# Kernel tuning notes

Hardware: AMD Instinct MI355X
Metric: run time of the kernel (lower is better)

The kernel has to match this reference:

```python
import jax, jax.numpy as jnp
import numpy as np

B, L, T = 32, 512, 400
EMB, PRE, ENC, ARNN, DRNN, NSYM = 512, 256, 512, 1024, 1024, 256
MEAN_COEFF, SCALE_COEFF = 1.0, 10.0


def setup_inputs() -> dict:
    key = jax.random.key(0)
    ks = jax.random.split(key, 20)
    s = 0.02
    inp = {
        'memory': jax.random.normal(ks[0], (B, L, ENC), jnp.float32),
        'decoder_inputs': jax.random.normal(ks[1], (B, EMB, T), jnp.float32),
        'memory_lengths': jax.random.randint(ks[2], (B,), L // 2, L + 1).astype(jnp.int64),
        # prenet
        'pW1': jax.random.normal(ks[3], (PRE, EMB), jnp.float32) * s,
        'pb1': jnp.zeros((PRE,), jnp.float32),
        'pW2': jax.random.normal(ks[4], (PRE, PRE), jnp.float32) * s,
        'pb2': jnp.zeros((PRE,), jnp.float32),
        # attention LSTMCell
        'aWih': jax.random.normal(ks[5], (4 * ARNN, PRE + ENC), jnp.float32) * s,
        'aWhh': jax.random.normal(ks[6], (4 * ARNN, ARNN), jnp.float32) * s,
        'abih': jnp.zeros((4 * ARNN,), jnp.float32),
        'abhh': jnp.zeros((4 * ARNN,), jnp.float32),
        # Gaussian attention param linear (weight zero-init in torch; small here)
        'attWp': jax.random.normal(ks[7], (2, ARNN), jnp.float32) * 0.001,
        'attbp': jnp.zeros((2,), jnp.float32),
        # decoder LSTMCell
        'dWih': jax.random.normal(ks[8], (4 * DRNN, ARNN + ENC), jnp.float32) * s,
        'dWhh': jax.random.normal(ks[9], (4 * DRNN, DRNN), jnp.float32) * s,
        'dbih': jnp.zeros((4 * DRNN,), jnp.float32),
        'dbhh': jnp.zeros((4 * DRNN,), jnp.float32),
        # output linear
        'oW': jax.random.normal(ks[10], (NSYM, DRNN + ENC), jnp.float32) * s,
        'ob': jnp.zeros((NSYM,), jnp.float32),
    }
    return inp


def _lstm_cell(x, h, c, Wih, Whh, bih, bhh):
    g = x @ Wih.T + bih + h @ Whh.T + bhh
    i, f, gg, o = jnp.split(g, 4, axis=-1)
    c = jax.nn.sigmoid(f) * c + jax.nn.sigmoid(i) * jnp.tanh(gg)
    h = jax.nn.sigmoid(o) * jnp.tanh(c)
    return h, c


def _decoder_core(memory, decoder_inputs, memory_lengths,
                  pW1, pb1, pW2, pb2,
                  aWih, aWhh, abih, abhh,
                  attWp, attbp,
                  dWih, dWhh, dbih, dbhh,
                  oW, ob):
    b = memory.shape[0]
    Lm = memory.shape[1]
    # go frame + time-major inputs -> prenet (dropout is identity in eval)
    x = jnp.transpose(decoder_inputs, (2, 0, 1))            # [T, B, EMB]
    x = jnp.concatenate([jnp.zeros((1, b, EMB), x.dtype), x], axis=0)  # [T+1, B, EMB]
    x = jax.nn.relu(x @ pW1.T + pb1)
    x = jax.nn.relu(x @ pW2.T + pb2)                        # [T+1, B, PRE]
    x = x[:T]                                               # loop runs T steps

    lin = jnp.arange(Lm, dtype=memory.dtype)[None, :]       # [1, L]
    pad_mask = lin >= memory_lengths[:, None].astype(memory.dtype)  # [B, L] True at pad

    def step(carry, x_t):
        ah, ac, dh, dc, ctx, mean = carry
        cell_in = jnp.concatenate([x_t, ctx], axis=1)
        ah, ac = _lstm_cell(cell_in, ah, ac, aWih, aWhh, abih, abhh)
        params = ah @ attWp.T + attbp                       # [B, 2]
        mean = mean + jnp.exp(params[:, 0:1]) * MEAN_COEFF  # [B, 1]
        scale = jnp.exp(params[:, 1:2]) * SCALE_COEFF       # [B, 1]
        Z = jnp.sqrt(2.0 * np.pi * scale ** 2)
        w = jnp.exp(-0.5 * (lin - mean) ** 2 / scale ** 2) / Z  # [B, L]
        w = jnp.where(pad_mask, 0.0, w)
        ctx = jnp.einsum('bl,bld->bd', w, memory)           # [B, ENC]
        dec_in = jnp.concatenate([ah, ctx], axis=1)
        dh, dc = _lstm_cell(dec_in, dh, dc, dWih, dWhh, dbih, dbhh)
        out = jnp.concatenate([dh, ctx], axis=1) @ oW.T + ob  # [B, NSYM]
        return (ah, ac, dh, dc, ctx, mean), (out, w, params)

    z = jnp.zeros
    carry0 = (z((b, ARNN)), z((b, ARNN)), z((b, DRNN)), z((b, DRNN)),
              z((b, ENC)), z((b, 1)))
    _, (logits, aligns, ps) = jax.lax.scan(step, carry0, x)
    # time-major -> [B, T, ...]
    return (jnp.transpose(logits, (1, 0, 2)),
            jnp.transpose(aligns, (1, 0, 2)),
            jnp.transpose(ps, (1, 0, 2)))


def reference(memory, decoder_inputs, memory_lengths,
              pW1, pb1, pW2, pb2,
              aWih, aWhh, abih, abhh,
              attWp, attbp,
              dWih, dWhh, dbih, dbhh,
              oW, ob):
    return _decoder_core(memory, decoder_inputs, memory_lengths,
                         pW1, pb1, pW2, pb2,
                         aWih, aWhh, abih, abhh,
                         attWp, attbp,
                         dWih, dWhh, dbih, dbhh,
                         oW, ob)
```

## Files before the change

kernel.cpp:

```cpp
#include <hip/hip_runtime.h>
#include <math.h>

#define Bsz   32
#define Lmem  512
#define Tsteps 400
#define EMBD  512
#define PRE   256
#define ENCD  512
#define ARNN  1024
#define DRNN  1024
#define NSYM  256

typedef _Float16 f16x8 __attribute__((ext_vector_type(8)));
typedef float    f32x4 __attribute__((ext_vector_type(4)));
typedef _Float16 half_t;

#define KA  (PRE + ENCD + ARNN)
#define KAQ (KA / 4)
#define NMA (KAQ / 32)
#define KD  (ARNN + ENCD + DRNN)
#define KDQ (KD / 4)
#define NMD (KDQ / 32)
#define LDA_A 1800
#define LDA_D 2568

__device__ __forceinline__ void st_agent_f16(half_t* p, half_t v) {
    __hip_atomic_store((unsigned short*)p, __builtin_bit_cast(unsigned short, v),
                       __ATOMIC_RELAXED, __HIP_MEMORY_SCOPE_AGENT);
}
__device__ __forceinline__ void st_agent_f32(float* p, float v) {
    __hip_atomic_store(p, v, __ATOMIC_RELAXED, __HIP_MEMORY_SCOPE_AGENT);
}
__device__ __forceinline__ void st_agent_u32(unsigned* p, unsigned v) {
    __hip_atomic_store(p, v, __ATOMIC_RELAXED, __HIP_MEMORY_SCOPE_AGENT);
}
__device__ __forceinline__ float ld_agent_f32(const float* p) {
    return __hip_atomic_load(p, __ATOMIC_RELAXED, __HIP_MEMORY_SCOPE_AGENT);
}
__device__ __forceinline__ unsigned ld_agent_u32(const unsigned* p) {
    return __hip_atomic_load(p, __ATOMIC_RELAXED, __HIP_MEMORY_SCOPE_AGENT);
}
__device__ __forceinline__ f16x8 ld_agent_f16x8(const half_t* p) {
    union { unsigned long long u[2]; f16x8 v; } c;
    c.u[0] = __hip_atomic_load((const unsigned long long*)p,
                               __ATOMIC_RELAXED, __HIP_MEMORY_SCOPE_AGENT);
    c.u[1] = __hip_atomic_load(((const unsigned long long*)p) + 1,
                               __ATOMIC_RELAXED, __HIP_MEMORY_SCOPE_AGENT);
    return c.v;
}
__device__ __forceinline__ void keep16(f16x8& v) { asm volatile("" : "+v"(v)); }

template<int KIH, int KHH>
__global__ __launch_bounds__(256) void conv_lstm_w(
    const float* __restrict__ Wih, const float* __restrict__ Whh,
    const float* __restrict__ bih, const float* __restrict__ bhh,
    half_t* __restrict__ Wcat, float* __restrict__ bsum)
{
    constexpr int K = KIH + KHH;
    const int j = blockIdx.x;
    const float* srcA = Wih + (size_t)j * KIH;
    const float* srcB = Whh + (size_t)j * KHH;
    half_t* dst = Wcat + (size_t)j * K;
    for (int k = threadIdx.x; k < KIH; k += 256) dst[k]       = (half_t)srcA[k];
    for (int k = threadIdx.x; k < KHH; k += 256) dst[KIH + k] = (half_t)srcB[k];
    if (threadIdx.x == 0) bsum[j] = bih[j] + bhh[j];
}

__global__ __launch_bounds__(256) void conv_mat(
    const float* __restrict__ src, half_t* __restrict__ dst, int n)
{
    for (int i = blockIdx.x * 256 + threadIdx.x; i < n; i += gridDim.x * 256)
        dst[i] = (half_t)src[i];
}

__global__ __launch_bounds__(256) void prenet_kernel(
    const float* __restrict__ din,
    const float* __restrict__ pW1, const float* __restrict__ pb1,
    const float* __restrict__ pW2, const float* __restrict__ pb2,
    half_t* __restrict__ xpre)
{
    __shared__ float xs[8][EMBD];
    __shared__ float h1s[8][PRE];
    const int tid = threadIdx.x;
    const int row0 = blockIdx.x * 8;

    for (int idx = tid; idx < 8 * EMBD; idx += 256) {
        int r = idx >> 9;
        int e = idx & 511;
        int rid = row0 + r;
        int t = rid >> 5;
        int b = rid & 31;
        float v = 0.f;
        if (t > 0) v = din[(size_t)b * EMBD * Tsteps + (size_t)e * Tsteps + (t - 1)];
        xs[r][e] = v;
    }
    __syncthreads();

    {
        float acc[8] = {0.f,0.f,0.f,0.f,0.f,0.f,0.f,0.f};
        const float* wr = pW1 + (size_t)tid * EMBD;
        for (int e = 0; e < EMBD; e += 4) {
            float4 wv = *(const float4*)(wr + e);
            #pragma unroll
            for (int r = 0; r < 8; ++r) {
                float4 xv = *(const float4*)&xs[r][e];
                acc[r] += wv.x * xv.x + wv.y * xv.y + wv.z * xv.z + wv.w * xv.w;
            }
        }
        float bias = pb1[tid];
        #pragma unroll
        for (int r = 0; r < 8; ++r) h1s[r][tid] = fmaxf(acc[r] + bias, 0.f);
    }
    __syncthreads();

    {
        float acc[8] = {0.f,0.f,0.f,0.f,0.f,0.f,0.f,0.f};
        const float* wr = pW2 + (size_t)tid * PRE;
        for (int e = 0; e < PRE; e += 4) {
            float4 wv = *(const float4*)(wr + e);
            #pragma unroll
            for (int r = 0; r < 8; ++r) {
                float4 xv = *(const float4*)&h1s[r][e];
                acc[r] += wv.x * xv.x + wv.y * xv.y + wv.z * xv.z + wv.w * xv.w;
            }
        }
        float bias = pb2[tid];
        #pragma unroll
        for (int r = 0; r < 8; ++r) {
            int rid = row0 + r;
            int t = rid >> 5;
            int b = rid & 31;
            xpre[(size_t)t * Bsz * PRE + (size_t)b * PRE + tid] =
                (half_t)fmaxf(acc[r] + bias, 0.f);
        }
    }
}

__device__ __forceinline__ void g_arrive(unsigned* flags, unsigned ph)
{
    asm volatile("s_waitcnt vmcnt(0)" ::: "memory");
    __syncthreads();
    if (threadIdx.x == 0)
        st_agent_u32(flags + blockIdx.x * 16, ph);
}
__device__ __forceinline__ void g_wait(unsigned* flags, unsigned ph)
{
    if (blockIdx.x < 16 && threadIdx.x < 16) {
        const unsigned* f = flags + (blockIdx.x * 16 + threadIdx.x) * 16;
        while (ld_agent_u32(f) < ph) __builtin_amdgcn_s_sleep(1);
        if (threadIdx.x == 0)
            st_agent_u32(flags + (256 + blockIdx.x) * 16, ph);
    }
    if (blockIdx.x == 0 && threadIdx.x < 16) {
        const unsigned* f2 = flags + (256 + threadIdx.x) * 16;
        while (ld_agent_u32(f2) < ph) __builtin_amdgcn_s_sleep(1);
        if (threadIdx.x == 0)
            st_agent_u32(flags + 272 * 16, ph);
    }
    if (threadIdx.x == 0) {
        const unsigned* g = flags + 272 * 16;
        while (ld_agent_u32(g) < ph) __builtin_amdgcn_s_sleep(1);
    }
    __syncthreads();
}

__global__ __launch_bounds__(512, 1) void decoder_persistent(
    const half_t* __restrict__ Wcat_a, const float* __restrict__ bsum_a,
    const half_t* __restrict__ Wcat_d, const float* __restrict__ bsum_d,
    const half_t* __restrict__ Wo, const float* __restrict__ ob,
    const half_t* __restrict__ xpre,
    const float* __restrict__ attWp, const float* __restrict__ attbp,
    const int* __restrict__ mlen, const half_t* __restrict__ mem16,
    half_t* __restrict__ ah0, half_t* __restrict__ ah1,
    half_t* __restrict__ dh0, half_t* __restrict__ dh1,
    half_t* __restrict__ ctx0, half_t* __restrict__ ctx1,
    float* __restrict__ mean0, float* __restrict__ mean1,
    float* __restrict__ logits, float* __restrict__ aligns,
    float* __restrict__ ps,
    unsigned* flags)
{
    const int blk   = blockIdx.x;
    const int tid   = threadIdx.x;
    const int wave  = tid >> 6;
    const int lane  = tid & 63;
    const int btile = wave & 1;
    const int kq    = wave >> 1;
    const int m15   = lane & 15;
    const int kh    = lane >> 4;
    const int u0    = blk << 2;
    const int bb    = (btile << 4) + m15;

    __shared__ __align__(16) half_t wAl[16 * LDA_A];
    __shared__ __align__(16) half_t wDl[16 * LDA_D];
    __shared__ float gredA[4][2][16][16];
    __shared__ float gredD[4][2][16][16];
    __shared__ float wsh[Lmem];
    __shared__ float lred[16][33];
    __shared__ float wred8[8][2];
    __shared__ float bc2[2];

    for (int g = tid; g < 16 * (KA / 8); g += 512) {
        int r = g / (KA / 8);
        int c = (g - r * (KA / 8)) * 8;
        int jr = (r >> 2) * 1024 + u0 + (r & 3);
        *(f16x8*)(wAl + r * LDA_A + c) = *(const f16x8*)(Wcat_a + (size_t)jr * KA + c);
    }
    for (int g = tid; g < 16 * (KD / 8); g += 512) {
        int r = g / (KD / 8);
        int c = (g - r * (KD / 8)) * 8;
        int jr = (r >> 2) * 1024 + u0 + (r & 3);
        *(f16x8*)(wDl + r * LDA_D + c) = *(const f16x8*)(Wcat_d + (size_t)jr * KD + c);
    }
    float bsA[4] = {0.f,0.f,0.f,0.f}, bsD[4] = {0.f,0.f,0.f,0.f};
    float cA = 0.f, cD = 0.f;
    if (tid < 128) {
        const int ul = tid >> 5;
        #pragma unroll
        for (int gi = 0; gi < 4; ++gi) bsA[gi] = bsum_a[gi * 1024 + u0 + ul];
    } else if (tid < 256) {
        const int ul = (tid - 128) >> 5;
        #pragma unroll
        for (int gi = 0; gi < 4; ++gi) bsD[gi] = bsum_d[gi * 1024 + u0 + ul];
    }
    const half_t* lA = wAl + m15 * LDA_A + kq * KAQ + (kh << 3);
    const half_t* lD = wDl + m15 * LDA_D + kq * KDQ + (kh << 3);
    __syncthreads();

    f16x8 bvA[NMA], bvD[NMD];
    {
        const half_t* s0 = xpre;
        #pragma unroll
        for (int i = 0; i < NMA; ++i) {
            const int kg = kq * KAQ + i * 32 + (kh << 3);
            if (kg < PRE)             bvA[i] = *(const f16x8*)(s0 + bb * PRE + kg);
            else if (kg < PRE + ENCD) bvA[i] = ld_agent_f16x8(ctx1 + bb * ENCD + (kg - PRE));
            else                      bvA[i] = ld_agent_f16x8(ah1 + bb * ARNN + (kg - PRE - ENCD));
        }
    }

    unsigned ph = 0;

    for (int t = 0; t <= Tsteps; ++t) {
        const int par = t & 1;
        half_t*       ah_cur  = par ? ah1 : ah0;
        half_t*       ctx_cur = par ? ctx1 : ctx0;
        const half_t* ctx_prv = par ? ctx0 : ctx1;
        float*        mn_cur  = par ? mean1 : mean0;
        const float*  mn_prv  = par ? mean0 : mean1;
        half_t*       dh_s    = par ? dh0 : dh1;

        if (t < Tsteps) {
            f32x4 accA = {0.f,0.f,0.f,0.f};
            #pragma unroll
            for (int i = 0; i < NMA; ++i) {
                f16x8 av = *(const f16x8*)(lA + i * 32);
                accA = __builtin_amdgcn_mfma_f32_16x16x32_f16(av, bvA[i], accA, 0, 0, 0);
            }
            #pragma unroll
            for (int r = 0; r < 4; ++r)
                gredA[kq][btile][(kh << 2) + r][m15] = accA[r];
        }
        if (t > 0) {
            f32x4 accD = {0.f,0.f,0.f,0.f};
            #pragma unroll
            for (int i = 0; i < NMD; ++i) {
                f16x8 av = *(const f16x8*)(lD + i * 32);
                accD = __builtin_amdgcn_mfma_f32_16x16x32_f16(av, bvD[i], accD, 0, 0, 0);
            }
            #pragma unroll
            for (int r = 0; r < 4; ++r)
                gredD[kq][btile][(kh << 2) + r][m15] = accD[r];
        }
        __syncthreads();
        if (tid < 128) {
            if (t < Tsteps) {
                const int ul = tid >> 5;
                const int bq = tid & 31;
                const int bt = bq >> 4;
                const int nn = bq & 15;
                float g[4];
                #pragma unroll
                for (int gi = 0; gi < 4; ++gi) {
                    const int mr = (gi << 2) + ul;
                    g[gi] = gredA[0][bt][mr][nn] + gredA[1][bt][mr][nn]
                          + gredA[2][bt][mr][nn] + gredA[3][bt][mr][nn] + bsA[gi];
                }
                float si = 1.f / (1.f + expf(-g[0]));
                float sf = 1.f / (1.f + expf(-g[1]));
                float so = 1.f / (1.f + expf(-g[3]));
                cA = sf * cA + si * tanhf(g[2]);
                st_agent_f16(&ah_cur[bq * 1024 + u0 + ul], (half_t)(so * tanhf(cA)));
            }
        } else if (tid < 256) {
            if (t > 0) {
                const int lt = tid - 128;
                const int ul = lt >> 5;
                const int bq = lt & 31;
                const int bt = bq >> 4;
                const int nn = bq & 15;
                float g[4];
                #pragma unroll
                for (int gi = 0; gi < 4; ++gi) {
                    const int mr = (gi << 2) + ul;
                    g[gi] = gredD[0][bt][mr][nn] + gredD[1][bt][mr][nn]
                          + gredD[2][bt][mr][nn] + gredD[3][bt][mr][nn] + bsD[gi];
                }
                float si = 1.f / (1.f + expf(-g[0]));
                float sf = 1.f / (1.f + expf(-g[1]));
                float so = 1.f / (1.f + expf(-g[3]));
                cD = sf * cD + si * tanhf(g[2]);
                st_agent_f16(&dh_s[bq * 1024 + u0 + ul], (half_t)(so * tanhf(cD)));
            }
        }
        ++ph; g_arrive(flags, ph); g_wait(flags, ph);

        if (t < Tsteps) {
            const int abt = blk >> 3;
            const int dt  = blk & 7;
            float p0, p1;
            {
                union { unsigned u; _Float16 h[2]; } a;
                a.u = ld_agent_u32((const unsigned*)(ah_cur + abt * ARNN + 2 * tid));
                float a0 = (float)a.h[0], a1 = (float)a.h[1];
                float2 w0 = *(const float2*)(attWp + 2 * tid);
                float2 w1 = *(const float2*)(attWp + ARNN + 2 * tid);
                p0 = a0 * w0.x + a1 * w0.y;
                p1 = a0 * w1.x + a1 * w1.y;
            }
            #pragma unroll
            for (int off = 32; off > 0; off >>= 1) {
                p0 += __shfl_down(p0, off, 64);
                p1 += __shfl_down(p1, off, 64);
            }
            if (lane == 0) { wred8[wave][0] = p0; wred8[wave][1] = p1; }
            __syncthreads();
            if (tid == 0) {
                float q0 = attbp[0], q1 = attbp[1];
                #pragma unroll
                for (int w = 0; w < 8; ++w) { q0 += wred8[w][0]; q1 += wred8[w][1]; }
                float mn = ld_agent_f32(&mn_prv[abt]) + expf(q0) * 1.0f;
                float sc = expf(q1) * 10.0f;
                if (dt == 0) {
                    st_agent_f32(&mn_cur[abt], mn);
                    st_agent_f32(&ps[(size_t)abt * Tsteps * 2 + (size_t)t * 2 + 0], q0);
                    st_agent_f32(&ps[(size_t)abt * Tsteps * 2 + (size_t)t * 2 + 1], q1);
                }
                bc2[0] = mn; bc2[1] = sc;
            }
            __syncthreads();
            const float mn = bc2[0], sc = bc2[1];
            const float inv_s = 1.f / sc;
            const float coef = 0.3989422804014327f * inv_s;
            const int len = mlen[abt];
            {
                float z = ((float)tid - mn) * inv_s;
                float wv = (tid < len) ? expf(-0.5f * z * z) * coef : 0.f;
                wsh[tid] = wv;
                if (dt == 0)
                    st_agent_f32(&aligns[(size_t)abt * Tsteps * Lmem + (size_t)t * Lmem + tid], wv);
            }
            __syncthreads();
            int lo = (int)fmaxf(0.f, floorf(mn - 9.f * sc));
            int hi = (int)fminf((float)len, ceilf(mn + 9.f * sc) + 1.f);
            const int d8 = (dt << 6) + (wave << 3);
            const half_t* mb = mem16 + (size_t)abt * Lmem * ENCD + d8;
            float acc[8] = {0.f,0.f,0.f,0.f,0.f,0.f,0.f,0.f};
            for (int l = lo + lane; l < hi; l += 64) {
                f16x8 mv = *(const f16x8*)(mb + (size_t)l * ENCD);
                float w = wsh[l];
                #pragma unroll
                for (int j = 0; j < 8; ++j) acc[j] += w * (float)mv[j];
            }
            #pragma unroll
            for (int off = 32; off > 0; off >>= 1) {
                #pragma unroll
                for (int j = 0; j < 8; ++j) acc[j] += __shfl_down(acc[j], off, 64);
            }
            if (lane == 0) {
                #pragma unroll
                for (int j = 0; j < 4; ++j) {
                    union { unsigned u; _Float16 h[2]; } pk;
                    pk.h[0] = (_Float16)acc[2 * j];
                    pk.h[1] = (_Float16)acc[2 * j + 1];
                    st_agent_u32((unsigned*)(ctx_cur + abt * ENCD + d8 + 2 * j), pk.u);
                }
            }
        }
        if (t > 0) {
            const int b_o = tid & 31;
            const int ks  = tid >> 5;
            const half_t* wrow = Wo + (size_t)blk * (DRNN + ENCD) + ks * 96;
            float outacc = 0.f;
            #pragma unroll
            for (int half = 0; half < 2; ++half) {
                f16x8 wv[6], av[6];
                #pragma unroll
                for (int c8 = 0; c8 < 6; ++c8) {
                    const int cc = half * 6 + c8;
                    const int k = ks * 96 + cc * 8;
                    wv[c8] = *(const f16x8*)(wrow + cc * 8);
                    const half_t* ap = (k < DRNN) ? (dh_s + b_o * DRNN + k)
                                                  : (ctx_prv + b_o * ENCD + (k - DRNN));
                    av[c8] = ld_agent_f16x8(ap);
                }
                #pragma unroll
                for (int c8 = 0; c8 < 6; ++c8)
                    #pragma unroll
                    for (int e = 0; e < 8; ++e)
                        outacc += (float)wv[c8][e] * (float)av[c8][e];
            }
            lred[ks][b_o] = outacc;
            __syncthreads();
            if (tid < 32) {
                float s = 0.f;
                #pragma unroll
                for (int q = 0; q < 16; ++q) s += lred[q][tid];
                st_agent_f32(&logits[(size_t)tid * Tsteps * NSYM + (size_t)(t - 1) * NSYM + blk],
                             s + ob[blk]);
            }
        }
        if (t < Tsteps) {
            ++ph; g_arrive(flags, ph);
            if (t + 1 < Tsteps) {
                const half_t* s0n = xpre + (size_t)(t + 1) * Bsz * PRE;
                #pragma unroll
                for (int i = 0; i < NMA; ++i) {
                    const int kg = kq * KAQ + i * 32 + (kh << 3);
                    if (kg < PRE)
                        bvA[i] = *(const f16x8*)(s0n + bb * PRE + kg);
                    else if (kg >= PRE + ENCD)
                        bvA[i] = ld_agent_f16x8(ah_cur + bb * ARNN + (kg - PRE - ENCD));
                }
            }
            #pragma unroll
            for (int i = 0; i < NMD; ++i) {
                const int kg = kq * KDQ + i * 32 + (kh << 3);
                if (kg < ARNN)
                    bvD[i] = ld_agent_f16x8(ah_cur + bb * ARNN + kg);
                else if (kg >= ARNN + ENCD)
                    bvD[i] = ld_agent_f16x8(dh_s + bb * DRNN + (kg - ARNN - ENCD));
            }
            #pragma unroll
            for (int i = 0; i < NMA; ++i) keep16(bvA[i]);
            #pragma unroll
            for (int i = 0; i < NMD; ++i) keep16(bvD[i]);
            g_wait(flags, ph);
            if (t + 1 < Tsteps) {
                #pragma unroll
                for (int i = 0; i < NMA; ++i) {
                    const int kg = kq * KAQ + i * 32 + (kh << 3);
                    if (kg >= PRE && kg < PRE + ENCD)
                        bvA[i] = ld_agent_f16x8(ctx_cur + bb * ENCD + (kg - PRE));
                }
            }
            #pragma unroll
            for (int i = 0; i < NMD; ++i) {
                const int kg = kq * KDQ + i * 32 + (kh << 3);
                if (kg >= ARNN && kg < ARNN + ENCD)
                    bvD[i] = ld_agent_f16x8(ctx_cur + bb * ENCD + (kg - ARNN));
            }
        }
    }
}

extern "C" void kernel_launch(void* const* d_in, const int* in_sizes, int n_in,
                              void* d_out, int out_size, void* d_ws, size_t ws_size,
                              hipStream_t stream)
{
    (void)in_sizes; (void)n_in; (void)out_size; (void)ws_size;
    const float* memory = (const float*)d_in[0];
    const float* din    = (const float*)d_in[1];
    const int*   mlen   = (const int*)d_in[2];
    const float* pW1    = (const float*)d_in[3];
    const float* pb1    = (const float*)d_in[4];
    const float* pW2    = (const float*)d_in[5];
    const float* pb2    = (const float*)d_in[6];
    const float* aWih   = (const float*)d_in[7];
    const float* aWhh   = (const float*)d_in[8];
    const float* abih   = (const float*)d_in[9];
    const float* abhh   = (const float*)d_in[10];
    const float* attWp  = (const float*)d_in[11];
    const float* attbp  = (const float*)d_in[12];
    const float* dWih   = (const float*)d_in[13];
    const float* dWhh   = (const float*)d_in[14];
    const float* dbih   = (const float*)d_in[15];
    const float* dbhh   = (const float*)d_in[16];
    const float* oW     = (const float*)d_in[17];
    const float* ob     = (const float*)d_in[18];

    float* logits = (float*)d_out;
    float* aligns = logits + (size_t)Bsz * Tsteps * NSYM;
    float* ps     = aligns + (size_t)Bsz * Tsteps * Lmem;

    char* base = (char*)d_ws;
    auto alloc = [&](size_t bytes) -> char* {
        char* p = base; base += (bytes + 255) & ~(size_t)255; return p;
    };
    half_t* Wcat_a = (half_t*)alloc((size_t)4096 * KA * 2);
    half_t* Wcat_d = (half_t*)alloc((size_t)4096 * KD * 2);
    half_t* Wo     = (half_t*)alloc((size_t)NSYM * (DRNN + ENCD) * 2);
    float*  bsum_a = (float*)alloc(4096 * 4);
    float*  bsum_d = (float*)alloc(4096 * 4);
    half_t* xpre   = (half_t*)alloc((size_t)Tsteps * Bsz * PRE * 2);
    half_t* mem16  = (half_t*)alloc((size_t)Bsz * Lmem * ENCD * 2);
    half_t* ah0    = (half_t*)alloc(Bsz * ARNN * 2);
    half_t* ah1    = (half_t*)alloc(Bsz * ARNN * 2);
    half_t* dh0    = (half_t*)alloc(Bsz * DRNN * 2);
    half_t* dh1    = (half_t*)alloc(Bsz * DRNN * 2);
    half_t* ctx0   = (half_t*)alloc(Bsz * ENCD * 2);
    half_t* ctx1   = (half_t*)alloc(Bsz * ENCD * 2);
    float*  mean0  = (float*)alloc(Bsz * 4);
    float*  mean1  = (float*)alloc(Bsz * 4);
    unsigned* flags = (unsigned*)alloc(288 * 16 * 4);

    (void)hipMemsetAsync(ah1,   0, Bsz * ARNN * 2, stream);
    (void)hipMemsetAsync(dh1,   0, Bsz * DRNN * 2, stream);
    (void)hipMemsetAsync(ctx1,  0, Bsz * ENCD * 2, stream);
    (void)hipMemsetAsync(mean0, 0, Bsz * 4, stream);
    (void)hipMemsetAsync(mean1, 0, Bsz * 4, stream);
    (void)hipMemsetAsync(flags, 0, 288 * 16 * 4, stream);

    conv_lstm_w<PRE + ENCD, ARNN><<<4096, 256, 0, stream>>>(
        aWih, aWhh, abih, abhh, Wcat_a, bsum_a);
    conv_lstm_w<ARNN + ENCD, DRNN><<<4096, 256, 0, stream>>>(
        dWih, dWhh, dbih, dbhh, Wcat_d, bsum_d);
    conv_mat<<<768, 256, 0, stream>>>(oW, Wo, NSYM * (DRNN + ENCD));
    conv_mat<<<4096, 256, 0, stream>>>(memory, mem16, Bsz * Lmem * ENCD);
    prenet_kernel<<<Tsteps * Bsz / 8, 256, 0, stream>>>(din, pW1, pb1, pW2, pb2, xpre);

    decoder_persistent<<<256, 512, 0, stream>>>(
        Wcat_a, bsum_a, Wcat_d, bsum_d, Wo, ob, xpre,
        attWp, attbp, mlen, mem16,
        ah0, ah1, dh0, dh1, ctx0, ctx1, mean0, mean1,
        logits, aligns, ps,
        flags);
}
```

Before: 15.22 ms.

## Pipeline output projection into LSTM phase and use grouped grid barrier

The output linear layer moves out of the post-attention phase and into the LSTM phase one step later, lagging by two steps and adding one extra loop iteration. The attention parameter dot product now runs as per-block partial sums written to a global buffer, so the attention phase no longer reloads the whole hidden vector. Align stores are split across the 8 blocks of a batch. The grid barrier becomes an 8-group, 32-per-group two-level tree, and launch bounds move to 2 waves per SIMD. Together these aim to shorten the serial critical path of each step, at the cost of more complex phase ordering and an extra pipeline iteration.

```diff
diff --git a/kernel.cpp b/kernel.cpp
--- a/kernel.cpp
+++ b/kernel.cpp
@@ -34,10 +34,16 @@
 __device__ __forceinline__ void st_agent_u32(unsigned* p, unsigned v) {
     __hip_atomic_store(p, v, __ATOMIC_RELAXED, __HIP_MEMORY_SCOPE_AGENT);
 }
+__device__ __forceinline__ void st_agent_u64(unsigned long long* p, unsigned long long v) {
+    __hip_atomic_store(p, v, __ATOMIC_RELAXED, __HIP_MEMORY_SCOPE_AGENT);
+}
 __device__ __forceinline__ float ld_agent_f32(const float* p) {
     return __hip_atomic_load(p, __ATOMIC_RELAXED, __HIP_MEMORY_SCOPE_AGENT);
 }
 __device__ __forceinline__ unsigned ld_agent_u32(const unsigned* p) {
+    return __hip_atomic_load(p, __ATOMIC_RELAXED, __HIP_MEMORY_SCOPE_AGENT);
+}
+__device__ __forceinline__ unsigned long long ld_agent_u64(const unsigned long long* p) {
     return __hip_atomic_load(p, __ATOMIC_RELAXED, __HIP_MEMORY_SCOPE_AGENT);
 }
 __device__ __forceinline__ f16x8 ld_agent_f16x8(const half_t* p) {
@@ -143,28 +149,31 @@
     if (threadIdx.x == 0)
         st_agent_u32(flags + blockIdx.x * 16, ph);
 }
-__device__ __forceinline__ void g_wait(unsigned* flags, unsigned ph)
-{
-    if (blockIdx.x < 16 && threadIdx.x < 16) {
-        const unsigned* f = flags + (blockIdx.x * 16 + threadIdx.x) * 16;
-        while (ld_agent_u32(f) < ph) __builtin_amdgcn_s_sleep(1);
+__device__ __forceinline__ void g_wait(unsigned* flags, unsigned ph, int grp, int grank)
+{
+    if (grank == 0) {
+        if (threadIdx.x < 32) {
+            const unsigned* f = flags + (grp * 32 + threadIdx.x) * 16;
+            while (ld_agent_u32(f) < ph) __builtin_amdgcn_s_sleep(1);
+        }
         if (threadIdx.x == 0)
-            st_agent_u32(flags + (256 + blockIdx.x) * 16, ph);
-    }
-    if (blockIdx.x == 0 && threadIdx.x < 16) {
-        const unsigned* f2 = flags + (256 + threadIdx.x) * 16;
-        while (ld_agent_u32(f2) < ph) __builtin_amdgcn_s_sleep(1);
+            st_agent_u32(flags + (256 + grp) * 16, ph);
+        if (threadIdx.x < 8) {
+            const unsigned* f2 = flags + (256 + threadIdx.x) * 16;
+            while (ld_agent_u32(f2) < ph) __builtin_amdgcn_s_sleep(1);
+        }
         if (threadIdx.x == 0)
-            st_agent_u32(flags + 272 * 16, ph);
-    }
-    if (threadIdx.x == 0) {
-        const unsigned* g = flags + 272 * 16;
-        while (ld_agent_u32(g) < ph) __builtin_amdgcn_s_sleep(1);
+            st_agent_u32(flags + (264 + grp) * 16, ph);
+    } else {
+        if (threadIdx.x == 0) {
+            const unsigned* g = flags + (264 + grp) * 16;
+            while (ld_agent_u32(g) < ph) __builtin_amdgcn_s_sleep(1);
+        }
     }
     __syncthreads();
 }
 
-__global__ __launch_bounds__(512, 1) void decoder_persistent(
+__global__ __launch_bounds__(512, 2) void decoder_persistent(
     const half_t* __restrict__ Wcat_a, const float* __restrict__ bsum_a,
     const half_t* __restrict__ Wcat_d, const float* __restrict__ bsum_d,
     const half_t* __restrict__ Wo, const float* __restrict__ ob,
@@ -175,6 +184,7 @@
     half_t* __restrict__ dh0, half_t* __restrict__ dh1,
     half_t* __restrict__ ctx0, half_t* __restrict__ ctx1,
     float* __restrict__ mean0, float* __restrict__ mean1,
+    float* __restrict__ partials,
     float* __restrict__ logits, float* __restrict__ aligns,
     float* __restrict__ ps,
     unsigned* flags)
@@ -189,6 +199,8 @@
     const int kh    = lane >> 4;
     const int u0    = blk << 2;
     const int bb    = (btile << 4) + m15;
+    const int grp   = blk >> 5;
+    const int grank = blk & 31;
 
     __shared__ __align__(16) half_t wAl[16 * LDA_A];
     __shared__ __align__(16) half_t wDl[16 * LDA_D];
@@ -196,6 +208,7 @@
     __shared__ float gredD[4][2][16][16];
     __shared__ float wsh[Lmem];
     __shared__ float lred[16][33];
+    __shared__ float part[4][32][2];
     __shared__ float wred8[8][2];
     __shared__ float bc2[2];
 
@@ -212,11 +225,14 @@
         *(f16x8*)(wDl + r * LDA_D + c) = *(const f16x8*)(Wcat_d + (size_t)jr * KD + c);
     }
     float bsA[4] = {0.f,0.f,0.f,0.f}, bsD[4] = {0.f,0.f,0.f,0.f};
+    float wp0 = 0.f, wp1 = 0.f;
     float cA = 0.f, cD = 0.f;
     if (tid < 128) {
         const int ul = tid >> 5;
         #pragma unroll
         for (int gi = 0; gi < 4; ++gi) bsA[gi] = bsum_a[gi * 1024 + u0 + ul];
+        wp0 = attWp[u0 + ul];
+        wp1 = attWp[ARNN + u0 + ul];
     } else if (tid < 256) {
         const int ul = (tid - 128) >> 5;
         #pragma unroll
@@ -240,14 +256,14 @@
 
     unsigned ph = 0;
 
-    for (int t = 0; t <= Tsteps; ++t) {
+    for (int t = 0; t <= Tsteps + 1; ++t) {
         const int par = t & 1;
         half_t*       ah_cur  = par ? ah1 : ah0;
         half_t*       ctx_cur = par ? ctx1 : ctx0;
-        const half_t* ctx_prv = par ? ctx0 : ctx1;
         float*        mn_cur  = par ? mean1 : mean0;
         const float*  mn_prv  = par ? mean0 : mean1;
         half_t*       dh_s    = par ? dh0 : dh1;
+        const half_t* dh_prv  = par ? dh1 : dh0;
 
         if (t < Tsteps) {
             f32x4 accA = {0.f,0.f,0.f,0.f};
@@ -260,7 +276,7 @@
             for (int r = 0; r < 4; ++r)
                 gredA[kq][btile][(kh << 2) + r][m15] = accA[r];
         }
-        if (t > 0) {
+        if (t >= 1 && t <= Tsteps) {
             f32x4 accD = {0.f,0.f,0.f,0.f};
             #pragma unroll
             for (int i = 0; i < NMD; ++i) {
@@ -270,6 +286,31 @@
             #pragma unroll
             for (int r = 0; r < 4; ++r)
                 gredD[kq][btile][(kh << 2) + r][m15] = accD[r];
+        }
+        if (t >= 2) {
+            const int b_o = tid & 31;
+            const int ks  = tid >> 5;
+            const half_t* wrow = Wo + (size_t)blk * (DRNN + ENCD) + ks * 96;
+            float outacc = 0.f;
+            #pragma unroll
+            for (int hf = 0; hf < 2; ++hf) {
+                f16x8 wv[6], av[6];
+                #pragma unroll
+                for (int c8 = 0; c8 < 6; ++c8) {
+                    const int cc = hf * 6 + c8;
+                    const int k = ks * 96 + cc * 8;
+                    wv[c8] = *(const f16x8*)(wrow + cc * 8);
+                    const half_t* ap = (k < DRNN) ? (dh_prv + b_o * DRNN + k)
+                                                  : (ctx_cur + b_o * ENCD + (k - DRNN));
+                    av[c8] = ld_agent_f16x8(ap);
+                }
+                #pragma unroll
+                for (int c8 = 0; c8 < 6; ++c8)
+                    #pragma unroll
+                    for (int e = 0; e < 8; ++e)
+                        outacc += (float)wv[c8][e] * (float)av[c8][e];
+            }
+            lred[ks][b_o] = outacc;
         }
         __syncthreads();
         if (tid < 128) {
@@ -289,10 +330,13 @@
                 float sf = 1.f / (1.f + expf(-g[1]));
                 float so = 1.f / (1.f + expf(-g[3]));
                 cA = sf * cA + si * tanhf(g[2]);
-                st_agent_f16(&ah_cur[bq * 1024 + u0 + ul], (half_t)(so * tanhf(cA)));
+                float hval = so * tanhf(cA);
+                st_agent_f16(&ah_cur[bq * 1024 + u0 + ul], (half_t)hval);
+                part[ul][bq][0] = hval * wp0;
+                part[ul][bq][1] = hval * wp1;
             }
         } else if (tid < 256) {
-            if (t > 0) {
+            if (t >= 1 && t <= Tsteps) {
                 const int lt = tid - 128;
                 const int ul = lt >> 5;
                 const int bq = lt & 31;
@@ -311,21 +355,34 @@
                 cD = sf * cD + si * tanhf(g[2]);
                 st_agent_f16(&dh_s[bq * 1024 + u0 + ul], (half_t)(so * tanhf(cD)));
             }
-        }
-        ++ph; g_arrive(flags, ph); g_wait(flags, ph);
+        } else if (tid < 288) {
+            if (t >= 2) {
+                const int b = tid - 256;
+                float s = 0.f;
+                #pragma unroll
+                for (int q = 0; q < 16; ++q) s += lred[q][b];
+                st_agent_f32(&logits[(size_t)b * Tsteps * NSYM + (size_t)(t - 2) * NSYM + blk],
+                             s + ob[blk]);
+            }
+        }
+        __syncthreads();
+        if (tid < 32 && t < Tsteps) {
+            float p0 = part[0][tid][0] + part[1][tid][0] + part[2][tid][0] + part[3][tid][0];
+            float p1 = part[0][tid][1] + part[1][tid][1] + part[2][tid][1] + part[3][tid][1];
+            union { float2 f; unsigned long long u; } pk;
+            pk.f.x = p0; pk.f.y = p1;
+            st_agent_u64((unsigned long long*)(partials + ((size_t)tid * 256 + blk) * 2), pk.u);
+        }
+        if (t <= Tsteps) { ++ph; g_arrive(flags, ph); g_wait(flags, ph, grp, grank); }
 
         if (t < Tsteps) {
             const int abt = blk >> 3;
             const int dt  = blk & 7;
-            float p0, p1;
-            {
-                union { unsigned u; _Float16 h[2]; } a;
-                a.u = ld_agent_u32((const unsigned*)(ah_cur + abt * ARNN + 2 * tid));
-                float a0 = (float)a.h[0], a1 = (float)a.h[1];
-                float2 w0 = *(const float2*)(attWp + 2 * tid);
-                float2 w1 = *(const float2*)(attWp + ARNN + 2 * tid);
-                p0 = a0 * w0.x + a1 * w0.y;
-                p1 = a0 * w1.x + a1 * w1.y;
+            float p0 = 0.f, p1 = 0.f;
+            if (tid < 256) {
+                union { unsigned long long u; float2 f; } pv;
+                pv.u = ld_agent_u64((const unsigned long long*)(partials + ((size_t)abt * 256 + tid) * 2));
+                p0 = pv.f.x; p1 = pv.f.y;
             }
             #pragma unroll
             for (int off = 32; off > 0; off >>= 1) {
@@ -354,12 +411,13 @@
             const int len = mlen[abt];
             {
                 float z = ((float)tid - mn) * inv_s;
-                float wv = (tid < len) ? expf(-0.5f * z * z) * coef : 0.f;
-                wsh[tid] = wv;
-                if (dt == 0)
-                    st_agent_f32(&aligns[(size_t)abt * Tsteps * Lmem + (size_t)t * Lmem + tid], wv);
+                wsh[tid] = (tid < len) ? expf(-0.5f * z * z) * coef : 0.f;
             }
             __syncthreads();
+            if (tid < 64) {
+                const int l = (dt << 6) + tid;
+                st_agent_f32(&aligns[(size_t)abt * Tsteps * Lmem + (size_t)t * Lmem + l], wsh[l]);
+            }
             int lo = (int)fmaxf(0.f, floorf(mn - 9.f * sc));
             int hi = (int)fminf((float)len, ceilf(mn + 9.f * sc) + 1.f);
             const int d8 = (dt << 6) + (wave << 3);
@@ -385,41 +443,7 @@
                     st_agent_u32((unsigned*)(ctx_cur + abt * ENCD + d8 + 2 * j), pk.u);
                 }
             }
-        }
-        if (t > 0) {
-            const int b_o = tid & 31;
-            const int ks  = tid >> 5;
-            const half_t* wrow = Wo + (size_t)blk * (DRNN + ENCD) + ks * 96;
-            float outacc = 0.f;
-            #pragma unroll
-            for (int half = 0; half < 2; ++half) {
-                f16x8 wv[6], av[6];
-                #pragma unroll
-                for (int c8 = 0; c8 < 6; ++c8) {
-                    const int cc = half * 6 + c8;
-                    const int k = ks * 96 + cc * 8;
-                    wv[c8] = *(const f16x8*)(wrow + cc * 8);
-                    const half_t* ap = (k < DRNN) ? (dh_s + b_o * DRNN + k)
-                                                  : (ctx_prv + b_o * ENCD + (k - DRNN));
-                    av[c8] = ld_agent_f16x8(ap);
-                }
-                #pragma unroll
-                for (int c8 = 0; c8 < 6; ++c8)
-                    #pragma unroll
-                    for (int e = 0; e < 8; ++e)
-                        outacc += (float)wv[c8][e] * (float)av[c8][e];
-            }
-            lred[ks][b_o] = outacc;
-            __syncthreads();
-            if (tid < 32) {
-                float s = 0.f;
-                #pragma unroll
-                for (int q = 0; q < 16; ++q) s += lred[q][tid];
-                st_agent_f32(&logits[(size_t)tid * Tsteps * NSYM + (size_t)(t - 1) * NSYM + blk],
-                             s + ob[blk]);
-            }
-        }
-        if (t < Tsteps) {
+
             ++ph; g_arrive(flags, ph);
             if (t + 1 < Tsteps) {
                 const half_t* s0n = xpre + (size_t)(t + 1) * Bsz * PRE;
@@ -444,7 +468,7 @@
             for (int i = 0; i < NMA; ++i) keep16(bvA[i]);
             #pragma unroll
             for (int i = 0; i < NMD; ++i) keep16(bvD[i]);
-            g_wait(flags, ph);
+            g_wait(flags, ph, grp, grank);
             if (t + 1 < Tsteps) {
                 #pragma unroll
                 for (int i = 0; i < NMA; ++i) {
@@ -511,14 +535,15 @@
     half_t* ctx1   = (half_t*)alloc(Bsz * ENCD * 2);
     float*  mean0  = (float*)alloc(Bsz * 4);
     float*  mean1  = (float*)alloc(Bsz * 4);
-    unsigned* flags = (unsigned*)alloc(288 * 16 * 4);
+    float*  partials = (float*)alloc((size_t)Bsz * 256 * 2 * 4);
+    unsigned* flags = (unsigned*)alloc(272 * 16 * 4);
 
     (void)hipMemsetAsync(ah1,   0, Bsz * ARNN * 2, stream);
     (void)hipMemsetAsync(dh1,   0, Bsz * DRNN * 2, stream);
     (void)hipMemsetAsync(ctx1,  0, Bsz * ENCD * 2, stream);
     (void)hipMemsetAsync(mean0, 0, Bsz * 4, stream);
     (void)hipMemsetAsync(mean1, 0, Bsz * 4, stream);
-    (void)hipMemsetAsync(flags, 0, 288 * 16 * 4, stream);
+    (void)hipMemsetAsync(flags, 0, 272 * 16 * 4, stream);
 
     conv_lstm_w<PRE + ENCD, ARNN><<<4096, 256, 0, stream>>>(
         aWih, aWhh, abih, abhh, Wcat_a, bsum_a);
@@ -531,7 +556,7 @@
     decoder_persistent<<<256, 512, 0, stream>>>(
         Wcat_a, bsum_a, Wcat_d, bsum_d, Wo, ob, xpre,
         attWp, attbp, mlen, mem16,
-        ah0, ah1, dh0, dh1, ctx0, ctx1, mean0, mean1,
+        ah0, ah1, dh0, dh1, ctx0, ctx1, mean0, mean1, partials,
         logits, aligns, ps,
         flags);
 }
```

Result: faster. 14.33 ms (-5.9%).
